# Kernel optimization log

Hardware: AMD Instinct MI355X
Metric: run time of the kernel (lower is better)

## Reference

```python
import jax, jax.numpy as jnp
import numpy as np

EPS = 1e-8  # torch F.cosine_similarity default eps


def setup_inputs() -> dict:
    key = jax.random.key(0)
    k1, k2 = jax.random.split(key)
    proto = jax.random.normal(k1, (1, 10, 640, 1, 196), dtype=jnp.float32)
    query = jax.random.normal(k2, (1, 300, 640, 1, 196), dtype=jnp.float32)
    return {"proto": proto, "query": query}


def reference(proto, query):
    # squeeze episode and singleton spatial dims: [way, C, N], [Q, C, N]
    p = proto[0, :, :, 0, :]
    q = query[0, :, :, 0, :]
    # cosine similarity over C between every proto spatial location i and
    # query spatial location j -> sim[q, w, i, j]
    # dots via a single contraction instead of the repeated/broadcast tensors
    dots = jnp.einsum('wci,qcj->qwij', p, q)               # [Q, way, N, N]
    p_norm = jnp.sqrt(jnp.sum(p * p, axis=1))              # [way, N]
    q_norm = jnp.sqrt(jnp.sum(q * q, axis=1))              # [Q, N]
    denom = p_norm[None, :, :, None] * q_norm[:, None, None, :]
    sim = dots / jnp.maximum(denom, EPS)
    return sim
```

## Files before the change

kernel.cpp:

```cpp
#include <hip/hip_runtime.h>
#include <stdint.h>

#define QN    300
#define WN    10
#define CD    640
#define IJ    196
#define MROWS 1960
#define NTOT  58800
#define OUTQ  384160
#define EPSV  1e-8f

#define BM    256
#define BN    256
#define BK    64
#define BUFE  ((BM + BN) * BK)
#define NTK   (CD / BK)

#define MT_TILES 8
#define NT_TILES 230
#define NWG      (MT_TILES * NT_TILES)
#define CPX      (NWG / 8)

typedef __attribute__((ext_vector_type(8))) short bf16x8;
typedef __attribute__((ext_vector_type(4))) float f32x4;

__device__ __forceinline__ unsigned short f2bf(float f) {
    uint32_t u = __float_as_uint(f);
    u += 0x7FFFu + ((u >> 16) & 1u);
    return (unsigned short)(u >> 16);
}

__device__ __forceinline__ void gload16(const void* g, void* l) {
    __builtin_amdgcn_global_load_lds(
        (const __attribute__((address_space(1))) void*)g,
        (__attribute__((address_space(3))) void*)l,
        16, 0, 0);
}

__global__ __launch_bounds__(256)
void prep_kernel(const float* __restrict__ X, uint4* __restrict__ XT,
                 float* __restrict__ nrm)
{
    __shared__ float T[128][21];
    __shared__ float ssL[16][17];

    const int b  = blockIdx.y;
    const int i0 = blockIdx.x * 16;
    const int t  = threadIdx.x;
    const float* Xb = X + (size_t)b * (CD * IJ);

    const int cA  = t >> 2;
    const int i4  = (t & 3) * 4;
    const int iv  = i0 + i4;
    const bool liv = (iv <= IJ - 4);

    const int il = t >> 4;
    const int u  = t & 15;
    float ss = 0.f;

    const int ig   = i0 + il;
    const bool wok = (ig < IJ);
    const int rowg = b * IJ + (wok ? ig : IJ - 1);
    const int uxor = rowg & 7;

    for (int cc = 0; cc < CD / 128; ++cc) {
        #pragma unroll
        for (int pass = 0; pass < 2; ++pass) {
            int cl = pass * 64 + cA;
            int c  = cc * 128 + cl;
            float4 v = make_float4(0.f, 0.f, 0.f, 0.f);
            if (liv) v = *(const float4*)&Xb[(size_t)c * IJ + iv];
            T[cl][i4 + 0] = v.x; T[cl][i4 + 1] = v.y;
            T[cl][i4 + 2] = v.z; T[cl][i4 + 3] = v.w;
        }
        __syncthreads();
        float v[8];
        #pragma unroll
        for (int r = 0; r < 8; ++r) { v[r] = T[u * 8 + r][il]; ss += v[r] * v[r]; }
        if (wok) {
            union { unsigned short s[8]; uint4 q; } pk;
            #pragma unroll
            for (int r = 0; r < 8; ++r) pk.s[r] = f2bf(v[r]);
            int us = (u & 8) | ((u & 7) ^ uxor);
            XT[(size_t)rowg * (CD / 8) + cc * 16 + us] = pk.q;
        }
        __syncthreads();
    }

    ssL[il][u] = ss;
    __syncthreads();
    if (t < 16) {
        int igw = i0 + t;
        if (igw < IJ) {
            float s = 0.f;
            #pragma unroll
            for (int k = 0; k < 16; ++k) s += ssL[t][k];
            nrm[b * IJ + igw] = sqrtf(s);
        }
    }
}

__global__ __launch_bounds__(512, 2)
void gemm_kernel(const uint4* __restrict__ AT, const uint4* __restrict__ BT,
                 const float* __restrict__ pn, const float* __restrict__ qn,
                 float* __restrict__ out)
{
    __shared__ unsigned short lds[2 * BUFE];

    const int bid = blockIdx.x;
    const int swz = (bid & 7) * CPX + (bid >> 3);
    const int mt  = swz & (MT_TILES - 1);
    const int nt  = swz >> 3;
    const int m0  = mt * BM;
    const int n0  = nt * BN;

    const int t  = threadIdx.x;
    const int w  = t >> 6, l = t & 63;
    const int fr = l & 15, fq = l >> 4;
    const int wm0 = (w >> 2) * 128;
    const int wn0 = (w & 3) * 64;

    const int lr = l >> 3, lu = l & 7;
    int ra00 = m0 +   0 + w * 8 + lr; if (ra00 > MROWS - 1) ra00 = MROWS - 1;
    int ra01 = m0 +  64 + w * 8 + lr; if (ra01 > MROWS - 1) ra01 = MROWS - 1;
    int ra10 = m0 + 128 + w * 8 + lr; if (ra10 > MROWS - 1) ra10 = MROWS - 1;
    int ra11 = m0 + 192 + w * 8 + lr; if (ra11 > MROWS - 1) ra11 = MROWS - 1;
    int rb00 = n0 +   0 + w * 8 + lr; if (rb00 > NTOT - 1) rb00 = NTOT - 1;
    int rb01 = n0 +  64 + w * 8 + lr; if (rb01 > NTOT - 1) rb01 = NTOT - 1;
    int rb10 = n0 + 128 + w * 8 + lr; if (rb10 > NTOT - 1) rb10 = NTOT - 1;
    int rb11 = n0 + 192 + w * 8 + lr; if (rb11 > NTOT - 1) rb11 = NTOT - 1;
    const uint4* ga00 = AT + (size_t)ra00 * 80 + lu;
    const uint4* ga01 = AT + (size_t)ra01 * 80 + lu;
    const uint4* ga10 = AT + (size_t)ra10 * 80 + lu;
    const uint4* ga11 = AT + (size_t)ra11 * 80 + lu;
    const uint4* gb00 = BT + (size_t)rb00 * 80 + lu;
    const uint4* gb01 = BT + (size_t)rb01 * 80 + lu;
    const uint4* gb10 = BT + (size_t)rb10 * 80 + lu;
    const uint4* gb11 = BT + (size_t)rb11 * 80 + lu;
    const int la00 = (  0 + w * 8) * 64;
    const int la01 = ( 64 + w * 8) * 64;
    const int la10 = (128 + w * 8) * 64;
    const int la11 = (192 + w * 8) * 64;
    const int lb00 = BM * 64 + (  0 + w * 8) * 64;
    const int lb01 = BM * 64 + ( 64 + w * 8) * 64;
    const int lb10 = BM * 64 + (128 + w * 8) * 64;
    const int lb11 = BM * 64 + (192 + w * 8) * 64;

    const int fqS0 = fq << 3;
    const int fqS1 = (fq + 4) << 3;
    int baA[8], kyA[8], baB[4], kyB[4];
    #pragma unroll
    for (int i = 0; i < 8; ++i) {
        int rowa = wm0 + i * 16 + fr;
        baA[i] = rowa * 64;  kyA[i] = (rowa & 7) << 3;
    }
    #pragma unroll
    for (int i = 0; i < 4; ++i) {
        int rowb = wn0 + i * 16 + fr;
        baB[i] = BM * 64 + rowb * 64;  kyB[i] = (rowb & 7) << 3;
    }

    f32x4 acc[8][4];
    #pragma unroll
    for (int a = 0; a < 8; ++a)
        #pragma unroll
        for (int bb = 0; bb < 4; ++bb)
            acc[a][bb] = (f32x4){0.f, 0.f, 0.f, 0.f};

#define ST2(PA, PB, LA, LB)                                               \
    gload16(PA, (char*)&lds[(LA)]); PA += 8;                              \
    gload16(PB, (char*)&lds[(LB)]); PB += 8;

#define RD_A(OC, G)                                                       \
    _Pragma("unroll")                                                     \
    for (int mm = 0; mm < 4; ++mm) {                                      \
        af[mm]   = *(const bf16x8*)&lds[(OC) + baA[(G)+mm]                \
                                        + (fqS0 ^ kyA[(G)+mm])];          \
        af[4+mm] = *(const bf16x8*)&lds[(OC) + baA[(G)+mm]                \
                                        + (fqS1 ^ kyA[(G)+mm])];          \
    }
#define RD_B(BV, OC, G)                                                   \
    _Pragma("unroll")                                                     \
    for (int nn = 0; nn < 2; ++nn) {                                      \
        BV[nn]   = *(const bf16x8*)&lds[(OC) + baB[(G)+nn]                \
                                        + (fqS0 ^ kyB[(G)+nn])];          \
        BV[2+nn] = *(const bf16x8*)&lds[(OC) + baB[(G)+nn]                \
                                        + (fqS1 ^ kyB[(G)+nn])];          \
    }
#define MF(MB, NB, BV)                                                    \
    _Pragma("unroll")                                                     \
    for (int ks = 0; ks < 2; ++ks)                                        \
        _Pragma("unroll")                                                 \
        for (int mm = 0; mm < 4; ++mm)                                    \
            _Pragma("unroll")                                             \
            for (int nn = 0; nn < 2; ++nn)                                \
                acc[(MB)+mm][(NB)+nn] =                                   \
                    __builtin_amdgcn_mfma_f32_16x16x32_bf16(              \
                        af[ks*4+mm], BV[ks*2+nn],                         \
                        acc[(MB)+mm][(NB)+nn], 0, 0, 0);

#define BAR    __builtin_amdgcn_s_barrier()
#define LGKM0  do { asm volatile("s_waitcnt lgkmcnt(0)" ::: "memory");    \
                    __builtin_amdgcn_sched_barrier(0); } while (0)
#define VMC(N) asm volatile("s_waitcnt vmcnt(" #N ")" ::: "memory")
#define PRIO1  __builtin_amdgcn_s_setprio(1)
#define PRIO0  __builtin_amdgcn_s_setprio(0)

    ST2(ga00, ga01, la00, la01);
    ST2(gb00, gb01, lb00, lb01);
    ST2(ga10, ga11, la10, la11);
    ST2(gb10, gb11, lb10, lb11);
    ST2(ga00, ga01, BUFE + la00, BUFE + la01);
    VMC(2); BAR;

    for (int i5 = 0; i5 < NTK / 2; ++i5) {
        bf16x8 af[8], b0[4], b1[4];
        RD_A(0, 0); RD_B(b0, 0, 0);
        ST2(gb00, gb01, BUFE + lb00, BUFE + lb01);
        BAR; LGKM0;
        PRIO1; MF(0, 0, b0); PRIO0;
        BAR;
        RD_B(b1, 0, 2);
        ST2(ga10, ga11, BUFE + la10, BUFE + la11);
        BAR; LGKM0;
        PRIO1; MF(0, 2, b1); PRIO0;
        BAR;
        RD_A(0, 4);
        ST2(gb10, gb11, BUFE + lb10, BUFE + lb11);
        BAR; LGKM0;
        PRIO1; MF(4, 2, b1); PRIO0;
        BAR;
        ST2(ga00, ga01, la00, la01);
        PRIO1; MF(4, 0, b0); PRIO0;
        VMC(2); BAR;
        RD_A(BUFE, 0); RD_B(b0, BUFE, 0);
        ST2(gb00, gb01, lb00, lb01);
        BAR; LGKM0;
        PRIO1; MF(0, 0, b0); PRIO0;
        BAR;
        RD_B(b1, BUFE, 2);
        ST2(ga10, ga11, la10, la11);
        BAR; LGKM0;
        PRIO1; MF(0, 2, b1); PRIO0;
        BAR;
        RD_A(BUFE, 4);
        ST2(gb10, gb11, lb10, lb11);
        BAR; LGKM0;
        PRIO1; MF(4, 2, b1); PRIO0;
        BAR;
        ST2(ga00, ga01, BUFE + la00, BUFE + la01);
        PRIO1; MF(4, 0, b0); PRIO0;
        VMC(2); BAR;
    }

    VMC(0);

#undef ST2
#undef RD_A
#undef RD_B
#undef MF
#undef BAR
#undef LGKM0
#undef VMC
#undef PRIO1
#undef PRIO0

    float  rqv[4];
    int    nvalid[4];
    size_t obase[4];
    #pragma unroll
    for (int tn = 0; tn < 4; ++tn) {
        int n = n0 + wn0 + tn * 16 + fr;
        nvalid[tn] = (n < NTOT);
        int nc = nvalid[tn] ? n : NTOT - 1;
        int q  = nc / IJ;
        int j  = nc - q * IJ;
        rqv[tn]   = qn[nc];
        obase[tn] = (size_t)q * OUTQ + j;
    }
    #pragma unroll
    for (int tm = 0; tm < 8; ++tm) {
        #pragma unroll
        for (int rr = 0; rr < 4; ++rr) {
            int m = m0 + wm0 + tm * 16 + fq * 4 + rr;
            if (m < MROWS) {
                float rp = pn[m];
                #pragma unroll
                for (int tn = 0; tn < 4; ++tn) {
                    if (nvalid[tn]) {
                        float d = fmaxf(rp * rqv[tn], EPSV);
                        out[obase[tn] + (size_t)m * IJ] =
                            acc[tm][tn][rr] * __builtin_amdgcn_rcpf(d);
                    }
                }
            }
        }
    }
}

#define BMF 128
#define BNF 224
#define LPAD 40
__global__ __launch_bounds__(512, 4)
void sim_fallback(const float* __restrict__ proto,
                  const float* __restrict__ query,
                  float* __restrict__ out)
{
    __shared__ unsigned short As[BMF][LPAD];
    __shared__ unsigned short Bs[BNF][LPAD];
    __shared__ float redA[4][BMF];
    __shared__ float redB[2][BNF];
    __shared__ float rpS[BMF];
    __shared__ float rqS[BNF];

    const int tid = threadIdx.x;
    const int m0  = blockIdx.x * BMF;
    const int q   = blockIdx.y;

    const int mA  = tid & (BMF - 1);
    const int krA = tid >> 7;
    const int wiA = m0 + mA;
    const bool va = (wiA < MROWS);
    const int wA  = va ? (wiA / IJ) : 0;
    const int iA  = va ? (wiA - wA * IJ) : 0;
    const float* pA = proto + wA * (CD * IJ) + iA;

    const bool tb  = (tid < 448);
    const int jB   = tb ? (tid % BNF) : 0;
    const int krB  = tb ? (tid / BNF) : 0;
    const bool vb  = tb && (jB < IJ);
    const float* qB = query + q * (CD * IJ) + jB;

    float ssA = 0.f, ssB = 0.f;

    const int wv   = tid >> 6;
    const int lane = tid & 63;
    const int wm0  = (wv >> 1) * 32;
    const int wn0  = (wv & 1) * 112;
    const int fr   = lane & 15;
    const int fq   = lane >> 4;

    f32x4 acc[2][7];
    #pragma unroll
    for (int a = 0; a < 2; a++)
        #pragma unroll
        for (int b = 0; b < 7; b++)
            acc[a][b] = (f32x4){0.f, 0.f, 0.f, 0.f};

    for (int it = 0; it < CD / 32; ++it) {
        const int c0 = it * 32;
        {
            float v[8];
            #pragma unroll
            for (int e = 0; e < 8; e++) {
                int c = c0 + krA * 8 + e;
                v[e] = va ? pA[c * IJ] : 0.f;
            }
            #pragma unroll
            for (int e = 0; e < 8; e++) ssA += v[e] * v[e];
            union { unsigned short s[8]; uint4 u; } pk;
            #pragma unroll
            for (int e = 0; e < 8; e++) pk.s[e] = f2bf(v[e]);
            *(uint4*)&As[mA][krA * 8] = pk.u;
        }
        if (tb) {
            #pragma unroll
            for (int h = 0; h < 2; ++h) {
                float v[8];
                #pragma unroll
                for (int e = 0; e < 8; e++) {
                    int c = c0 + krB * 16 + h * 8 + e;
                    v[e] = vb ? qB[c * IJ] : 0.f;
                }
                #pragma unroll
                for (int e = 0; e < 8; e++) ssB += v[e] * v[e];
                union { unsigned short s[8]; uint4 u; } pk;
                #pragma unroll
                for (int e = 0; e < 8; e++) pk.s[e] = f2bf(v[e]);
                *(uint4*)&Bs[jB][krB * 16 + h * 8] = pk.u;
            }
        }
        __syncthreads();
        bf16x8 af[2], bfv[7];
        #pragma unroll
        for (int tm = 0; tm < 2; tm++)
            af[tm] = *(const bf16x8*)&As[wm0 + tm * 16 + fr][fq * 8];
        #pragma unroll
        for (int tn = 0; tn < 7; tn++)
            bfv[tn] = *(const bf16x8*)&Bs[wn0 + tn * 16 + fr][fq * 8];
        #pragma unroll
        for (int tm = 0; tm < 2; tm++)
            #pragma unroll
            for (int tn = 0; tn < 7; tn++)
                acc[tm][tn] = __builtin_amdgcn_mfma_f32_16x16x32_bf16(
                    af[tm], bfv[tn], acc[tm][tn], 0, 0, 0);
        __syncthreads();
    }

    redA[krA][mA] = ssA;
    if (tb) redB[krB][jB] = ssB;
    __syncthreads();
    if (tid < BMF) {
        rpS[tid] = sqrtf(redA[0][tid] + redA[1][tid] + redA[2][tid] + redA[3][tid]);
    } else if (tid >= 256 && tid < 256 + BNF) {
        int j = tid - 256;
        rqS[j] = sqrtf(redB[0][j] + redB[1][j]);
    }
    __syncthreads();

    #pragma unroll
    for (int tm = 0; tm < 2; tm++) {
        #pragma unroll
        for (int tn = 0; tn < 7; tn++) {
            #pragma unroll
            for (int r = 0; r < 4; r++) {
                int rl = wm0 + tm * 16 + fq * 4 + r;
                int cl = wn0 + tn * 16 + fr;
                int wi = m0 + rl;
                if (wi < MROWS && cl < IJ) {
                    float denom = fmaxf(rpS[rl] * rqS[cl], 1e-8f);
                    out[(size_t)(q * MROWS + wi) * IJ + cl] = acc[tm][tn][r] / denom;
                }
            }
        }
    }
}

extern "C" void kernel_launch(void* const* d_in, const int* in_sizes, int n_in,
                              void* d_out, int out_size, void* d_ws, size_t ws_size,
                              hipStream_t stream) {
    const float* proto = (const float*)d_in[0];
    const float* query = (const float*)d_in[1];
    float* out = (float*)d_out;

    const size_t off_pT = 0;
    const size_t off_qT = 2508800;
    const size_t off_pn = 77772800;
    const size_t off_qn = 77780736;
    const size_t need   = 78015936;

    if (ws_size < need) {
        dim3 grid((MROWS + BMF - 1) / BMF, QN);
        sim_fallback<<<grid, 512, 0, stream>>>(proto, query, out);
        return;
    }

    char* ws = (char*)d_ws;
    uint4* pT = (uint4*)(ws + off_pT);
    uint4* qT = (uint4*)(ws + off_qT);
    float* pn = (float*)(ws + off_pn);
    float* qn = (float*)(ws + off_qn);

    prep_kernel<<<dim3(13, QN), 256, 0, stream>>>(query, qT, qn);
    prep_kernel<<<dim3(13, WN), 256, 0, stream>>>(proto, pT, pn);

    gemm_kernel<<<dim3(NWG), 512, 0, stream>>>(pT, qT, pn, qn, out);
}
```

Before: 393.0 us.

## Transpose MFMA accumulators for float4 output stores and drop redundant barriers

Swaps the MFMA A/B operands so each lane's four accumulator values lie along consecutive query columns. The epilogue can then load query norms as float4 and write output as float4 vectors instead of scalar strided stores. This targets the large fp32 output write traffic. Separately, it removes three intermediate workgroup barriers per half-iteration in the main loop to cut synchronization stalls. That relies on the remaining barriers being enough to order LDS reuse safely.

```diff
diff --git a/kernel.cpp b/kernel.cpp
--- a/kernel.cpp
+++ b/kernel.cpp
@@ -196,7 +196,7 @@
             for (int nn = 0; nn < 2; ++nn)                                \
                 acc[(MB)+mm][(NB)+nn] =                                   \
                     __builtin_amdgcn_mfma_f32_16x16x32_bf16(              \
-                        af[ks*4+mm], BV[ks*2+nn],                         \
+                        BV[ks*2+nn], af[ks*4+mm],                         \
                         acc[(MB)+mm][(NB)+nn], 0, 0, 0);
 
 #define BAR    __builtin_amdgcn_s_barrier()
@@ -219,17 +219,14 @@
         ST2(gb00, gb01, BUFE + lb00, BUFE + lb01);
         BAR; LGKM0;
         PRIO1; MF(0, 0, b0); PRIO0;
-        BAR;
         RD_B(b1, 0, 2);
         ST2(ga10, ga11, BUFE + la10, BUFE + la11);
         BAR; LGKM0;
         PRIO1; MF(0, 2, b1); PRIO0;
-        BAR;
         RD_A(0, 4);
         ST2(gb10, gb11, BUFE + lb10, BUFE + lb11);
         BAR; LGKM0;
         PRIO1; MF(4, 2, b1); PRIO0;
-        BAR;
         ST2(ga00, ga01, la00, la01);
         PRIO1; MF(4, 0, b0); PRIO0;
         VMC(2); BAR;
@@ -237,17 +234,14 @@
         ST2(gb00, gb01, lb00, lb01);
         BAR; LGKM0;
         PRIO1; MF(0, 0, b0); PRIO0;
-        BAR;
         RD_B(b1, BUFE, 2);
         ST2(ga10, ga11, la10, la11);
         BAR; LGKM0;
         PRIO1; MF(0, 2, b1); PRIO0;
-        BAR;
         RD_A(BUFE, 4);
         ST2(gb10, gb11, lb10, lb11);
         BAR; LGKM0;
         PRIO1; MF(4, 2, b1); PRIO0;
-        BAR;
         ST2(ga00, ga01, BUFE + la00, BUFE + la01);
         PRIO1; MF(4, 0, b0); PRIO0;
         VMC(2); BAR;
@@ -265,33 +259,34 @@
 #undef PRIO1
 #undef PRIO0
 
-    float  rqv[4];
-    int    nvalid[4];
-    size_t obase[4];
+    float4 rqv4[4];
+    int    nok[4];
+    size_t ob[4];
     #pragma unroll
     for (int tn = 0; tn < 4; ++tn) {
-        int n = n0 + wn0 + tn * 16 + fr;
-        nvalid[tn] = (n < NTOT);
-        int nc = nvalid[tn] ? n : NTOT - 1;
+        int n = n0 + wn0 + tn * 16 + fq * 4;
+        nok[tn] = (n < NTOT);
+        int nc = nok[tn] ? n : NTOT - 4;
         int q  = nc / IJ;
         int j  = nc - q * IJ;
-        rqv[tn]   = qn[nc];
-        obase[tn] = (size_t)q * OUTQ + j;
+        rqv4[tn] = *(const float4*)&qn[nc];
+        ob[tn] = (size_t)q * OUTQ + j;
     }
     #pragma unroll
     for (int tm = 0; tm < 8; ++tm) {
-        #pragma unroll
-        for (int rr = 0; rr < 4; ++rr) {
-            int m = m0 + wm0 + tm * 16 + fq * 4 + rr;
-            if (m < MROWS) {
-                float rp = pn[m];
-                #pragma unroll
-                for (int tn = 0; tn < 4; ++tn) {
-                    if (nvalid[tn]) {
-                        float d = fmaxf(rp * rqv[tn], EPSV);
-                        out[obase[tn] + (size_t)m * IJ] =
-                            acc[tm][tn][rr] * __builtin_amdgcn_rcpf(d);
-                    }
+        int m = m0 + wm0 + tm * 16 + fr;
+        if (m < MROWS) {
+            float rp = pn[m];
+            #pragma unroll
+            for (int tn = 0; tn < 4; ++tn) {
+                if (nok[tn]) {
+                    f32x4 a = acc[tm][tn];
+                    float4 o;
+                    o.x = a[0] * __builtin_amdgcn_rcpf(fmaxf(rp * rqv4[tn].x, EPSV));
+                    o.y = a[1] * __builtin_amdgcn_rcpf(fmaxf(rp * rqv4[tn].y, EPSV));
+                    o.z = a[2] * __builtin_amdgcn_rcpf(fmaxf(rp * rqv4[tn].z, EPSV));
+                    o.w = a[3] * __builtin_amdgcn_rcpf(fmaxf(rp * rqv4[tn].w, EPSV));
+                    *(float4*)&out[ob[tn] + (size_t)m * IJ] = o;
                 }
             }
         }
```

Result: faster. 352.0 us (-10.4%).
